# Kernel optimization log

Hardware: AMD Instinct MI355X
Metric: run time of the kernel (lower is better)

## Reference

```python
import jax, jax.numpy as jnp
import numpy as np

CDIM = 256  # part_size for energy_pooling_mask


def setup_inputs() -> dict:
    key = jax.random.key(0)
    ks = jax.random.split(key, 6)
    B, T, IDIM, HDIM, ODIM = 8, 2048, 512, 2048, 512
    x = jax.random.normal(ks[0], (B, T, IDIM), dtype=jnp.float32)
    mask_prev = jax.random.randint(ks[1], (B, T, HDIM), 0, 2, dtype=jnp.int32)
    W_enc = jax.random.normal(ks[2], (HDIM, IDIM), dtype=jnp.float32) * 0.02
    b_enc = jax.random.normal(ks[3], (HDIM,), dtype=jnp.float32) * 0.02
    W_dec = jax.random.normal(ks[4], (ODIM, HDIM), dtype=jnp.float32) * 0.02
    b_dec = jax.random.normal(ks[5], (ODIM,), dtype=jnp.float32) * 0.02
    return {"x": x, "mask_prev": mask_prev, "W_enc": W_enc, "b_enc": b_enc,
            "W_dec": W_dec, "b_dec": b_dec}


def _energy_pooling_mask(h, part_size):
    # topk over channel (last) dim of h^2; share=True -> k = 2*part_size
    B, T, H = h.shape
    k2 = 2 * part_size
    _, idx = jax.lax.top_k(h * h, k2)            # [B, T, 2c] unique indices
    idx_f = idx.reshape(B * T, k2)
    rows = jnp.arange(B * T)[:, None]
    base = jnp.zeros((B * T, H), dtype=h.dtype)
    # sum of one-hots over unique indices == scatter-set of 1.0
    mask_share = base.at[rows, idx_f].set(1.0).reshape(B, T, H)
    mask_cur = base.at[rows, idx_f[:, :part_size]].set(1.0).reshape(B, T, H)
    return mask_cur, mask_share


def reference(x, mask_prev, W_enc, b_enc, W_dec, b_dec):
    # encoder: Linear(idim -> hdim)
    h = jnp.einsum('bti,hi->bth', x, W_enc) + b_enc
    # hidden_exclude_activation with mask_prev given:
    # h[mask_prev.bool()] = 0
    mp = mask_prev.astype(h.dtype)
    h = jnp.where(mp > 0, jnp.zeros((), h.dtype), h)
    mask_cur, mask_cur_share = _energy_pooling_mask(h, CDIM)
    mask_prev_new = mp + mask_cur
    # h.masked_fill(~mask_cur_share.bool(), 0)
    h = h * mask_cur_share
    # decoder_src: Linear(hdim -> odim)
    out = jnp.einsum('bth,oh->bto', h, W_dec) + b_dec
    return out, mask_prev_new
```

## Files before the change

kernel.cpp:

```cpp
#include <hip/hip_runtime.h>
#include <hip/hip_bf16.h>

typedef __attribute__((ext_vector_type(8))) __bf16 bf16x8;
typedef __attribute__((ext_vector_type(4))) float f32x4;

#define MDIM 16384
#define HDIM 2048
#define IDIM 512
#define ODIM 512
#define CAP 768

static __device__ __forceinline__ unsigned short f2bf(float f) {
  unsigned int u = __float_as_uint(f);
  unsigned int r = (u + 0x7fffu + ((u >> 16) & 1u)) >> 16;
  return (unsigned short)r;
}

__global__ void cvt_bf16_kernel(const float* __restrict__ src,
                                unsigned short* __restrict__ dst, int n) {
  int i = (blockIdx.x * 256 + threadIdx.x) * 4;
  if (i >= n) return;
  float4 v = *(const float4*)(src + i);
  unsigned int a = (unsigned int)f2bf(v.x) | ((unsigned int)f2bf(v.y) << 16);
  unsigned int b = (unsigned int)f2bf(v.z) | ((unsigned int)f2bf(v.w) << 16);
  uint2 st; st.x = a; st.y = b;
  *(uint2*)(dst + i) = st;
}

__global__ __launch_bounds__(256) void gemm1_kernel(
    const float* __restrict__ x,
    const float* __restrict__ wenc,
    const float* __restrict__ benc,
    float* __restrict__ h) {
  __shared__ __align__(16) float As[32][132];
  __shared__ __align__(16) float Bs[32][132];
  const int t = threadIdx.x;
  const int tx = t & 15, ty = t >> 4;
  const int m0 = blockIdx.y * 128;
  const int n0 = blockIdx.x * 128;
  const int r0 = t >> 1;
  const int kh = (t & 1) * 16;

  const float* pa = x + (size_t)(m0 + r0) * IDIM + kh;
  const float* pb = wenc + (size_t)(n0 + r0) * IDIM + kh;

  float acc[8][8];
#pragma unroll
  for (int i = 0; i < 8; ++i)
#pragma unroll
    for (int j = 0; j < 8; ++j) acc[i][j] = 0.f;

  for (int kt = 0; kt < IDIM; kt += 32) {
    float4 a0 = *(const float4*)(pa + kt);
    float4 a1 = *(const float4*)(pa + kt + 4);
    float4 a2 = *(const float4*)(pa + kt + 8);
    float4 a3 = *(const float4*)(pa + kt + 12);
    float4 b0 = *(const float4*)(pb + kt);
    float4 b1 = *(const float4*)(pb + kt + 4);
    float4 b2 = *(const float4*)(pb + kt + 8);
    float4 b3 = *(const float4*)(pb + kt + 12);
    __syncthreads();
    {
      const float* aa = (const float*)&a0;
      const float av[16] = {a0.x, a0.y, a0.z, a0.w, a1.x, a1.y, a1.z, a1.w,
                            a2.x, a2.y, a2.z, a2.w, a3.x, a3.y, a3.z, a3.w};
      const float bv[16] = {b0.x, b0.y, b0.z, b0.w, b1.x, b1.y, b1.z, b1.w,
                            b2.x, b2.y, b2.z, b2.w, b3.x, b3.y, b3.z, b3.w};
      (void)aa;
#pragma unroll
      for (int j = 0; j < 16; ++j) {
        As[kh + j][r0] = av[j];
        Bs[kh + j][r0] = bv[j];
      }
    }
    __syncthreads();
#pragma unroll
    for (int k = 0; k < 32; ++k) {
      float4 av0 = *(const float4*)&As[k][ty * 4];
      float4 av1 = *(const float4*)&As[k][64 + ty * 4];
      float4 bv0 = *(const float4*)&Bs[k][tx * 4];
      float4 bv1 = *(const float4*)&Bs[k][64 + tx * 4];
      float am[8] = {av0.x, av0.y, av0.z, av0.w, av1.x, av1.y, av1.z, av1.w};
      float bm[8] = {bv0.x, bv0.y, bv0.z, bv0.w, bv1.x, bv1.y, bv1.z, bv1.w};
#pragma unroll
      for (int i = 0; i < 8; ++i)
#pragma unroll
        for (int j = 0; j < 8; ++j) acc[i][j] += am[i] * bm[j];
    }
  }
  float4 be0 = *(const float4*)(benc + n0 + tx * 4);
  float4 be1 = *(const float4*)(benc + n0 + 64 + tx * 4);
  float bb[8] = {be0.x, be0.y, be0.z, be0.w, be1.x, be1.y, be1.z, be1.w};
#pragma unroll
  for (int i = 0; i < 8; ++i) {
    int m = m0 + ((i < 4) ? (ty * 4 + i) : (64 + ty * 4 + (i - 4)));
    float* hrow = h + (size_t)m * HDIM + n0;
    float4 s0 = {acc[i][0] + bb[0], acc[i][1] + bb[1], acc[i][2] + bb[2], acc[i][3] + bb[3]};
    float4 s1 = {acc[i][4] + bb[4], acc[i][5] + bb[5], acc[i][6] + bb[6], acc[i][7] + bb[7]};
    *(float4*)(hrow + tx * 4) = s0;
    *(float4*)(hrow + 64 + tx * 4) = s1;
  }
}

__global__ __launch_bounds__(256) void select_kernel(
    float* __restrict__ hbuf,
    const int* __restrict__ maskp,
    unsigned short* __restrict__ hs) {
  const int row = blockIdx.x;
  const int t = threadIdx.x;
  const int lane = t & 63;
  const int w = t >> 6;
  __shared__ int hist[4096];
  __shared__ unsigned int cand512[CAP];
  __shared__ unsigned int cand256[CAP];
  __shared__ int scal[16];
  __shared__ int n512, n256;

  float* hrow = hbuf + (size_t)row * HDIM;
  const int* mrow = maskp + (size_t)row * HDIM;
  float hv[8];
  *(float4*)&hv[0] = *(const float4*)(hrow + t * 8);
  *(float4*)&hv[4] = *(const float4*)(hrow + t * 8 + 4);
  int4 mp0 = *(const int4*)(mrow + t * 8);
  int4 mp1 = *(const int4*)(mrow + t * 8 + 4);
  int mm[8] = {mp0.x, mp0.y, mp0.z, mp0.w, mp1.x, mp1.y, mp1.z, mp1.w};
#pragma unroll
  for (int i = 0; i < 8; ++i) hv[i] = (mm[i] > 0) ? 0.f : hv[i];
  unsigned int key[8];
#pragma unroll
  for (int i = 0; i < 8; ++i) key[i] = __float_as_uint(hv[i] * hv[i]);

#pragma unroll
  for (int i = 0; i < 16; ++i) hist[t + i * 256] = 0;
  if (t == 0) {
    n512 = 0; n256 = 0;
    scal[0] = 0; scal[1] = 0x40000000;
    scal[2] = 0; scal[3] = 0x40000000;
  }
  __syncthreads();
#pragma unroll
  for (int i = 0; i < 8; ++i)
    if (key[i]) atomicAdd(&hist[key[i] >> 20], 1);
  __syncthreads();

  if (w == 0) {
    const int base = lane * 64;
    int s = 0;
#pragma unroll
    for (int i = 0; i < 64; i += 4) {
      int4 hh = *(const int4*)&hist[base + i];
      s += hh.x + hh.y + hh.z + hh.w;
    }
    int rs = s;
#pragma unroll
    for (int d = 1; d < 64; d <<= 1) {
      int o = __shfl_down(rs, d, 64);
      rs += (lane + d < 64) ? o : 0;
    }
    int c = rs - s;
    for (int i = 60; i >= 0; i -= 4) {
      int4 hh = *(const int4*)&hist[base + i];
      int q[4] = {hh.x, hh.y, hh.z, hh.w};
#pragma unroll
      for (int j = 3; j >= 0; --j) {
        int hc = q[j];
        if (c < 512 && c + hc >= 512) { scal[0] = base + i + j; scal[1] = 512 - c; }
        if (c < 256 && c + hc >= 256) { scal[2] = base + i + j; scal[3] = 256 - c; }
        c += hc;
      }
    }
  }
  __syncthreads();
  const int b512 = scal[0], b256 = scal[2];
#pragma unroll
  for (int i = 0; i < 8; ++i) {
    if (key[i]) {
      int bin = (int)(key[i] >> 20);
      if (bin == b512) { int p = atomicAdd(&n512, 1); if (p < CAP) cand512[p] = key[i]; }
      if (bin == b256) { int p = atomicAdd(&n256, 1); if (p < CAP) cand256[p] = key[i]; }
    }
  }
  __syncthreads();

  if (w < 2) {
    const unsigned int bb = (unsigned int)scal[w * 2];
    const int r = scal[w * 2 + 1];
    const unsigned int* cand = w ? cand256 : cand512;
    int C = w ? n256 : n512;
    C = (C < CAP) ? C : CAP;
    unsigned int v = 0;
    if (r <= C) {
      v = bb << 20;
      for (int bit = 19; bit >= 0; --bit) {
        unsigned int cth = v | (1u << bit);
        int cnt = 0;
        for (int p = lane; p < C; p += 64) cnt += (cand[p] >= cth) ? 1 : 0;
#pragma unroll
        for (int d = 1; d < 64; d <<= 1) cnt += __shfl_xor(cnt, d, 64);
        if (cnt >= r) v = cth;
      }
    }
    if (lane == 0) scal[4 + w] = (int)v;
  }
  __syncthreads();
  const unsigned int v512 = (unsigned int)scal[4];
  const unsigned int v256 = (unsigned int)scal[5];

  int g = 0;
#pragma unroll
  for (int i = 0; i < 8; ++i) {
    g += (key[i] > v512) ? 1 : 0;
    g += (key[i] > v256) ? (1 << 16) : 0;
  }
#pragma unroll
  for (int d = 1; d < 64; d <<= 1) g += __shfl_xor(g, d, 64);
  if (lane == 0) scal[8 + w] = g;
  __syncthreads();
  g = scal[8] + scal[9] + scal[10] + scal[11];
  const int r512 = 512 - (g & 0xffff);
  const int r256 = 256 - (g >> 16);

  int tc = 0;
#pragma unroll
  for (int i = 0; i < 8; ++i) {
    tc += (key[i] == v512) ? 1 : 0;
    tc += (key[i] == v256) ? (1 << 16) : 0;
  }
  int sc = tc;
#pragma unroll
  for (int d = 1; d < 64; d <<= 1) {
    int o = __shfl_up(sc, d, 64);
    if (lane >= d) sc += o;
  }
  if (lane == 63) scal[12 + w] = sc;
  __syncthreads();
  int excl = sc - tc;
  for (int i = 0; i < w; ++i) excl += scal[12 + i];
  int run512 = excl & 0xffff;
  int run256 = (excl >> 16) & 0xffff;

  float mpn[8];
  unsigned int hb[4];
#pragma unroll
  for (int i = 0; i < 8; ++i) {
    bool share, cur;
    if (key[i] > v512) share = true;
    else if (key[i] == v512) { share = (run512 < r512); run512++; }
    else share = false;
    if (key[i] > v256) cur = true;
    else if (key[i] == v256) { cur = (run256 < r256); run256++; }
    else cur = false;
    mpn[i] = (float)mm[i] + (cur ? 1.0f : 0.0f);
    unsigned short bbits = f2bf(share ? hv[i] : 0.0f);
    if (i & 1) hb[i >> 1] |= ((unsigned int)bbits << 16);
    else hb[i >> 1] = (unsigned int)bbits;
  }
  float4 s0 = {mpn[0], mpn[1], mpn[2], mpn[3]};
  float4 s1 = {mpn[4], mpn[5], mpn[6], mpn[7]};
  *(float4*)(hrow + t * 8) = s0;
  *(float4*)(hrow + t * 8 + 4) = s1;
  uint4 hstore = {hb[0], hb[1], hb[2], hb[3]};
  *(uint4*)(hs + (size_t)row * HDIM + t * 8) = hstore;
}

__global__ __launch_bounds__(256) void gemm2_kernel(
    const unsigned short* __restrict__ A,
    const unsigned short* __restrict__ B,
    const float* __restrict__ bdec,
    float* __restrict__ out) {
  __shared__ __align__(16) __bf16 As[64 * 32];
  __shared__ __align__(16) __bf16 Bs[128 * 32];
  const int t = threadIdx.x;
  const int lane = t & 63;
  const int w = t >> 6;
  const int wm = w >> 1, wn = w & 1;
  const int m0 = blockIdx.y * 64;
  const int n0 = blockIdx.x * 128;
  const int r = t >> 2;
  const int k8 = (t & 3) * 8;

  f32x4 acc[2][4];
#pragma unroll
  for (int i = 0; i < 2; ++i)
#pragma unroll
    for (int j = 0; j < 4; ++j) acc[i][j] = (f32x4){0.f, 0.f, 0.f, 0.f};

  const int la = lane & 15;
  const int kq = (lane >> 4) * 8;

  for (int kt = 0; kt < HDIM; kt += 32) {
    uint4 a0 = *(const uint4*)(A + (size_t)(m0 + r) * HDIM + kt + k8);
    uint4 b0 = *(const uint4*)(B + (size_t)(n0 + r) * HDIM + kt + k8);
    uint4 b1 = *(const uint4*)(B + (size_t)(n0 + 64 + r) * HDIM + kt + k8);
    __syncthreads();
    *(uint4*)&As[r * 32 + k8] = a0;
    *(uint4*)&Bs[r * 32 + k8] = b0;
    *(uint4*)&Bs[(64 + r) * 32 + k8] = b1;
    __syncthreads();
    bf16x8 af[2], bg[4];
#pragma unroll
    for (int mi = 0; mi < 2; ++mi)
      af[mi] = *(const bf16x8*)&As[(wm * 32 + mi * 16 + la) * 32 + kq];
#pragma unroll
    for (int ni = 0; ni < 4; ++ni)
      bg[ni] = *(const bf16x8*)&Bs[(wn * 64 + ni * 16 + la) * 32 + kq];
#pragma unroll
    for (int mi = 0; mi < 2; ++mi)
#pragma unroll
      for (int ni = 0; ni < 4; ++ni)
        acc[mi][ni] = __builtin_amdgcn_mfma_f32_16x16x32_bf16(
            af[mi], bg[ni], acc[mi][ni], 0, 0, 0);
  }
  const int rq = (lane >> 4) * 4;
#pragma unroll
  for (int mi = 0; mi < 2; ++mi) {
#pragma unroll
    for (int ni = 0; ni < 4; ++ni) {
      int n = n0 + wn * 64 + ni * 16 + la;
      float bd = bdec[n];
#pragma unroll
      for (int rr = 0; rr < 4; ++rr) {
        int m = m0 + wm * 32 + mi * 16 + rq + rr;
        out[(size_t)m * ODIM + n] = acc[mi][ni][rr] + bd;
      }
    }
  }
}

extern "C" void kernel_launch(void* const* d_in, const int* in_sizes, int n_in,
                              void* d_out, int out_size, void* d_ws, size_t ws_size,
                              hipStream_t stream) {
  const float* x = (const float*)d_in[0];
  const int* mask_prev = (const int*)d_in[1];
  const float* W_enc = (const float*)d_in[2];
  const float* b_enc = (const float*)d_in[3];
  const float* W_dec = (const float*)d_in[4];
  const float* b_dec = (const float*)d_in[5];

  float* out = (float*)d_out;
  float* hbuf = out + (size_t)MDIM * ODIM;
  unsigned short* hs = (unsigned short*)d_ws;
  unsigned short* wdec = hs + (size_t)MDIM * HDIM;

  cvt_bf16_kernel<<<dim3((ODIM * HDIM) / (256 * 4)), dim3(256), 0, stream>>>(
      W_dec, wdec, ODIM * HDIM);
  gemm1_kernel<<<dim3(HDIM / 128, MDIM / 128), dim3(256), 0, stream>>>(
      x, W_enc, b_enc, hbuf);
  select_kernel<<<dim3(MDIM), dim3(256), 0, stream>>>(hbuf, mask_prev, hs);
  gemm2_kernel<<<dim3(ODIM / 128, MDIM / 64), dim3(256), 0, stream>>>(
      hs, wdec, b_dec, out);
}
```

Baseline: 837.7 us.

## Replace FP32 encoder GEMM with split-fp16 MFMA and exact-fp32 boundary refinement

Replaces the scalar FP32 SIMT encoder GEMM with an MFMA fp16 GEMM that emulates fp32 accuracy by splitting each operand into high and low fp16 parts along a concatenated K of 1536 (three products). The select kernel then finds channels whose energy lies within a small band around the top-k thresholds, recomputes those channels in exact fp32 from x and W_enc, and re-solves the thresholds so selection ties match the reference. The aim is to remove the FP32 CUDA-core bottleneck of the first GEMM. In exchange it adds two split kernels, extra workspace traffic (B_cat temporarily stored in the output buffer), and a per-row refinement step. Correctness depends on the candidate cap of 64 and on the band width.

```diff
diff --git a/kernel.cpp b/kernel.cpp
--- a/kernel.cpp
+++ b/kernel.cpp
@@ -2,13 +2,16 @@
 #include <hip/hip_bf16.h>
 
 typedef __attribute__((ext_vector_type(8))) __bf16 bf16x8;
+typedef __attribute__((ext_vector_type(8))) _Float16 f16x8;
 typedef __attribute__((ext_vector_type(4))) float f32x4;
 
 #define MDIM 16384
 #define HDIM 2048
 #define IDIM 512
 #define ODIM 512
+#define KCAT 1536
 #define CAP 768
+#define CAPC 64
 
 static __device__ __forceinline__ unsigned short f2bf(float f) {
   unsigned int u = __float_as_uint(f);
@@ -27,84 +30,131 @@
   *(uint2*)(dst + i) = st;
 }
 
-__global__ __launch_bounds__(256) void gemm1_kernel(
+static __device__ __forceinline__ void split_pack(const float4 v, uint2* h2, uint2* l2) {
+  float vv[4] = {v.x, v.y, v.z, v.w};
+  unsigned int hp[2], lp[2];
+#pragma unroll
+  for (int j = 0; j < 4; ++j) {
+    _Float16 hh = (_Float16)vv[j];
+    float back = (float)hh;
+    _Float16 ll = (_Float16)((vv[j] - back) * 2048.0f);
+    unsigned short hb = __builtin_bit_cast(unsigned short, hh);
+    unsigned short lb = __builtin_bit_cast(unsigned short, ll);
+    if (j & 1) { hp[j >> 1] |= (unsigned int)hb << 16; lp[j >> 1] |= (unsigned int)lb << 16; }
+    else       { hp[j >> 1] = hb; lp[j >> 1] = lb; }
+  }
+  h2->x = hp[0]; h2->y = hp[1];
+  l2->x = lp[0]; l2->y = lp[1];
+}
+
+__global__ void split_a_kernel(const float* __restrict__ src,
+                               unsigned short* __restrict__ dst) {
+  int idx = (blockIdx.x * 256 + threadIdx.x) * 4;
+  int row = idx >> 9, col = idx & 511;
+  uint2 h2, l2;
+  split_pack(*(const float4*)(src + idx), &h2, &l2);
+  unsigned short* drow = dst + (size_t)row * KCAT;
+  *(uint2*)(drow + col) = h2;
+  *(uint2*)(drow + 512 + col) = l2;
+  *(uint2*)(drow + 1024 + col) = h2;
+}
+
+__global__ void split_b_kernel(const float* __restrict__ src,
+                               unsigned short* __restrict__ dst) {
+  int idx = (blockIdx.x * 256 + threadIdx.x) * 4;
+  int row = idx >> 9, col = idx & 511;
+  uint2 h2, l2;
+  split_pack(*(const float4*)(src + idx), &h2, &l2);
+  unsigned short* drow = dst + (size_t)row * KCAT;
+  *(uint2*)(drow + col) = h2;
+  *(uint2*)(drow + 512 + col) = h2;
+  *(uint2*)(drow + 1024 + col) = l2;
+}
+
+__global__ __launch_bounds__(512) void gemm1_mfma_kernel(
+    const unsigned short* __restrict__ A,
+    const unsigned short* __restrict__ B,
+    const float* __restrict__ benc,
+    float* __restrict__ h) {
+  __shared__ __align__(16) _Float16 As[128 * 32];
+  __shared__ __align__(16) _Float16 Bs[128 * 32];
+  const int t = threadIdx.x;
+  const int lane = t & 63;
+  const int w = t >> 6;
+  const int wm = w >> 2;
+  const int wn = w & 3;
+  const int m0 = blockIdx.y * 128;
+  const int n0 = blockIdx.x * 128;
+  const int r = t >> 2;
+  const int k8 = (t & 3) * 8;
+
+  f32x4 acc1[4][2], acc2[4][2];
+#pragma unroll
+  for (int i = 0; i < 4; ++i)
+#pragma unroll
+    for (int j = 0; j < 2; ++j) {
+      acc1[i][j] = (f32x4){0.f, 0.f, 0.f, 0.f};
+      acc2[i][j] = (f32x4){0.f, 0.f, 0.f, 0.f};
+    }
+
+  const int la = lane & 15;
+  const int kq = (lane >> 4) * 8;
+  const unsigned short* pa = A + (size_t)(m0 + r) * KCAT + k8;
+  const unsigned short* pb = B + (size_t)(n0 + r) * KCAT + k8;
+
+  for (int kt = 0; kt < KCAT; kt += 32) {
+    uint4 av = *(const uint4*)(pa + kt);
+    uint4 bv = *(const uint4*)(pb + kt);
+    __syncthreads();
+    *(uint4*)&As[r * 32 + k8] = av;
+    *(uint4*)&Bs[r * 32 + k8] = bv;
+    __syncthreads();
+    f16x8 af[4], bg[2];
+#pragma unroll
+    for (int mi = 0; mi < 4; ++mi)
+      af[mi] = *(const f16x8*)&As[(wm * 64 + mi * 16 + la) * 32 + kq];
+#pragma unroll
+    for (int ni = 0; ni < 2; ++ni)
+      bg[ni] = *(const f16x8*)&Bs[(wn * 32 + ni * 16 + la) * 32 + kq];
+    if (kt < 512) {
+#pragma unroll
+      for (int mi = 0; mi < 4; ++mi)
+#pragma unroll
+        for (int ni = 0; ni < 2; ++ni)
+          acc1[mi][ni] = __builtin_amdgcn_mfma_f32_16x16x32_f16(
+              af[mi], bg[ni], acc1[mi][ni], 0, 0, 0);
+    } else {
+#pragma unroll
+      for (int mi = 0; mi < 4; ++mi)
+#pragma unroll
+        for (int ni = 0; ni < 2; ++ni)
+          acc2[mi][ni] = __builtin_amdgcn_mfma_f32_16x16x32_f16(
+              af[mi], bg[ni], acc2[mi][ni], 0, 0, 0);
+    }
+  }
+  const int rq = (lane >> 4) * 4;
+  const float eps = 1.0f / 2048.0f;
+#pragma unroll
+  for (int mi = 0; mi < 4; ++mi) {
+#pragma unroll
+    for (int ni = 0; ni < 2; ++ni) {
+      int n = n0 + wn * 32 + ni * 16 + la;
+      float bd = benc[n];
+#pragma unroll
+      for (int rr = 0; rr < 4; ++rr) {
+        int m = m0 + wm * 64 + mi * 16 + rq + rr;
+        h[(size_t)m * HDIM + n] = acc1[mi][ni][rr] + acc2[mi][ni][rr] * eps + bd;
+      }
+    }
+  }
+}
+
+__global__ __launch_bounds__(256) void select_kernel(
+    float* __restrict__ hbuf,
+    const int* __restrict__ maskp,
     const float* __restrict__ x,
     const float* __restrict__ wenc,
     const float* __restrict__ benc,
-    float* __restrict__ h) {
-  __shared__ __align__(16) float As[32][132];
-  __shared__ __align__(16) float Bs[32][132];
-  const int t = threadIdx.x;
-  const int tx = t & 15, ty = t >> 4;
-  const int m0 = blockIdx.y * 128;
-  const int n0 = blockIdx.x * 128;
-  const int r0 = t >> 1;
-  const int kh = (t & 1) * 16;
-
-  const float* pa = x + (size_t)(m0 + r0) * IDIM + kh;
-  const float* pb = wenc + (size_t)(n0 + r0) * IDIM + kh;
-
-  float acc[8][8];
-#pragma unroll
-  for (int i = 0; i < 8; ++i)
-#pragma unroll
-    for (int j = 0; j < 8; ++j) acc[i][j] = 0.f;
-
-  for (int kt = 0; kt < IDIM; kt += 32) {
-    float4 a0 = *(const float4*)(pa + kt);
-    float4 a1 = *(const float4*)(pa + kt + 4);
-    float4 a2 = *(const float4*)(pa + kt + 8);
-    float4 a3 = *(const float4*)(pa + kt + 12);
-    float4 b0 = *(const float4*)(pb + kt);
-    float4 b1 = *(const float4*)(pb + kt + 4);
-    float4 b2 = *(const float4*)(pb + kt + 8);
-    float4 b3 = *(const float4*)(pb + kt + 12);
-    __syncthreads();
-    {
-      const float* aa = (const float*)&a0;
-      const float av[16] = {a0.x, a0.y, a0.z, a0.w, a1.x, a1.y, a1.z, a1.w,
-                            a2.x, a2.y, a2.z, a2.w, a3.x, a3.y, a3.z, a3.w};
-      const float bv[16] = {b0.x, b0.y, b0.z, b0.w, b1.x, b1.y, b1.z, b1.w,
-                            b2.x, b2.y, b2.z, b2.w, b3.x, b3.y, b3.z, b3.w};
-      (void)aa;
-#pragma unroll
-      for (int j = 0; j < 16; ++j) {
-        As[kh + j][r0] = av[j];
-        Bs[kh + j][r0] = bv[j];
-      }
-    }
-    __syncthreads();
-#pragma unroll
-    for (int k = 0; k < 32; ++k) {
-      float4 av0 = *(const float4*)&As[k][ty * 4];
-      float4 av1 = *(const float4*)&As[k][64 + ty * 4];
-      float4 bv0 = *(const float4*)&Bs[k][tx * 4];
-      float4 bv1 = *(const float4*)&Bs[k][64 + tx * 4];
-      float am[8] = {av0.x, av0.y, av0.z, av0.w, av1.x, av1.y, av1.z, av1.w};
-      float bm[8] = {bv0.x, bv0.y, bv0.z, bv0.w, bv1.x, bv1.y, bv1.z, bv1.w};
-#pragma unroll
-      for (int i = 0; i < 8; ++i)
-#pragma unroll
-        for (int j = 0; j < 8; ++j) acc[i][j] += am[i] * bm[j];
-    }
-  }
-  float4 be0 = *(const float4*)(benc + n0 + tx * 4);
-  float4 be1 = *(const float4*)(benc + n0 + 64 + tx * 4);
-  float bb[8] = {be0.x, be0.y, be0.z, be0.w, be1.x, be1.y, be1.z, be1.w};
-#pragma unroll
-  for (int i = 0; i < 8; ++i) {
-    int m = m0 + ((i < 4) ? (ty * 4 + i) : (64 + ty * 4 + (i - 4)));
-    float* hrow = h + (size_t)m * HDIM + n0;
-    float4 s0 = {acc[i][0] + bb[0], acc[i][1] + bb[1], acc[i][2] + bb[2], acc[i][3] + bb[3]};
-    float4 s1 = {acc[i][4] + bb[4], acc[i][5] + bb[5], acc[i][6] + bb[6], acc[i][7] + bb[7]};
-    *(float4*)(hrow + tx * 4) = s0;
-    *(float4*)(hrow + 64 + tx * 4) = s1;
-  }
-}
-
-__global__ __launch_bounds__(256) void select_kernel(
-    float* __restrict__ hbuf,
-    const int* __restrict__ maskp,
     unsigned short* __restrict__ hs) {
   const int row = blockIdx.x;
   const int t = threadIdx.x;
@@ -113,8 +163,11 @@
   __shared__ int hist[4096];
   __shared__ unsigned int cand512[CAP];
   __shared__ unsigned int cand256[CAP];
-  __shared__ int scal[16];
-  __shared__ int n512, n256;
+  __shared__ float xrow[IDIM];
+  __shared__ int cidx[2][CAPC];
+  __shared__ float cex[2][CAPC];
+  __shared__ int scal[24];
+  __shared__ int n512, n256, ncnt0, ncnt1;
 
   float* hrow = hbuf + (size_t)row * HDIM;
   const int* mrow = maskp + (size_t)row * HDIM;
@@ -130,10 +183,12 @@
 #pragma unroll
   for (int i = 0; i < 8; ++i) key[i] = __float_as_uint(hv[i] * hv[i]);
 
+  *(float2*)&xrow[t * 2] = *(const float2*)(x + (size_t)row * IDIM + t * 2);
+
 #pragma unroll
   for (int i = 0; i < 16; ++i) hist[t + i * 256] = 0;
   if (t == 0) {
-    n512 = 0; n256 = 0;
+    n512 = 0; n256 = 0; ncnt0 = 0; ncnt1 = 0;
     scal[0] = 0; scal[1] = 0x40000000;
     scal[2] = 0; scal[3] = 0x40000000;
   }
@@ -203,8 +258,81 @@
     if (lane == 0) scal[4 + w] = (int)v;
   }
   __syncthreads();
+  const unsigned int v512a = (unsigned int)scal[4];
+  const unsigned int v256a = (unsigned int)scal[5];
+
+  const float vf0 = __uint_as_float(v512a), vf1 = __uint_as_float(v256a);
+  const bool act0 = (v512a != 0), act1 = (v256a != 0);
+  const float wd0 = 1e-4f * sqrtf(vf0) + 1e-12f;
+  const float wd1 = 1e-4f * sqrtf(vf1) + 1e-12f;
+  const float hi0 = vf0 + wd0, lo0 = vf0 - wd0;
+  const float hi1 = vf1 + wd1, lo1 = vf1 - wd1;
+  int gf = 0;
+#pragma unroll
+  for (int i = 0; i < 8; ++i) {
+    float kf = __uint_as_float(key[i]);
+    if (act0) {
+      if (kf > hi0) gf += 1;
+      else if (kf >= lo0) { int p = atomicAdd(&ncnt0, 1); if (p < CAPC) cidx[0][p] = t * 8 + i; }
+    }
+    if (act1) {
+      if (kf > hi1) gf += (1 << 16);
+      else if (kf >= lo1) { int p = atomicAdd(&ncnt1, 1); if (p < CAPC) cidx[1][p] = t * 8 + i; }
+    }
+  }
+#pragma unroll
+  for (int d = 1; d < 64; d <<= 1) gf += __shfl_xor(gf, d, 64);
+  if (lane == 0) scal[16 + w] = gf;
+  __syncthreads();
+  const int gft = scal[16] + scal[17] + scal[18] + scal[19];
+  const int t0n = (ncnt0 < CAPC) ? ncnt0 : CAPC;
+  const int t1n = (ncnt1 < CAPC) ? ncnt1 : CAPC;
+
+  if (w < 2) {
+    const int n = w ? t1n : t0n;
+    if (lane < n) {
+      const int ch = cidx[w][lane];
+      const float* wr = wenc + (size_t)ch * IDIM;
+      float s = 0.f;
+      for (int k = 0; k < IDIM; ++k) s = fmaf(xrow[k], wr[k], s);
+      cex[w][lane] = s + benc[ch];
+    }
+  }
+  __syncthreads();
+
+  if (w < 2) {
+    const bool act = w ? act1 : act0;
+    const int n = w ? t1n : t0n;
+    if (act && n > 0) {
+      int rr = (w ? 256 : 512) - (w ? (gft >> 16) : (gft & 0xffff));
+      rr = (rr < 1) ? 1 : ((rr > n) ? n : rr);
+      unsigned int v = 0;
+      for (int b = 31; b >= 0; --b) {
+        unsigned int cth = v | (1u << b);
+        int cnt = 0;
+        for (int j = lane; j < n; j += 64) {
+          float q = cex[w][j];
+          cnt += (__float_as_uint(q * q) >= cth) ? 1 : 0;
+        }
+#pragma unroll
+        for (int d = 1; d < 64; d <<= 1) cnt += __shfl_xor(cnt, d, 64);
+        if (cnt >= rr) v = cth;
+      }
+      if (lane == 0) scal[4 + w] = (int)v;
+    }
+  }
+  __syncthreads();
   const unsigned int v512 = (unsigned int)scal[4];
   const unsigned int v256 = (unsigned int)scal[5];
+
+  for (int j = 0; j < t0n; ++j) {
+    int ch = cidx[0][j];
+    if ((ch >> 3) == t) { float e = cex[0][j]; hv[ch & 7] = e; key[ch & 7] = __float_as_uint(e * e); }
+  }
+  for (int j = 0; j < t1n; ++j) {
+    int ch = cidx[1][j];
+    if ((ch >> 3) == t) { float e = cex[1][j]; hv[ch & 7] = e; key[ch & 7] = __float_as_uint(e * e); }
+  }
 
   int g = 0;
 #pragma unroll
@@ -339,14 +467,19 @@
 
   float* out = (float*)d_out;
   float* hbuf = out + (size_t)MDIM * ODIM;
+  unsigned short* acat = (unsigned short*)d_ws;
   unsigned short* hs = (unsigned short*)d_ws;
   unsigned short* wdec = hs + (size_t)MDIM * HDIM;
-
-  cvt_bf16_kernel<<<dim3((ODIM * HDIM) / (256 * 4)), dim3(256), 0, stream>>>(
+  unsigned short* bcat = (unsigned short*)d_out;
+
+  split_a_kernel<<<dim3((MDIM * IDIM) / 1024), dim3(256), 0, stream>>>(x, acat);
+  split_b_kernel<<<dim3((HDIM * IDIM) / 1024), dim3(256), 0, stream>>>(W_enc, bcat);
+  cvt_bf16_kernel<<<dim3((ODIM * HDIM) / 1024), dim3(256), 0, stream>>>(
       W_dec, wdec, ODIM * HDIM);
-  gemm1_kernel<<<dim3(HDIM / 128, MDIM / 128), dim3(256), 0, stream>>>(
-      x, W_enc, b_enc, hbuf);
-  select_kernel<<<dim3(MDIM), dim3(256), 0, stream>>>(hbuf, mask_prev, hs);
+  gemm1_mfma_kernel<<<dim3(HDIM / 128, MDIM / 128), dim3(512), 0, stream>>>(
+      acat, bcat, b_enc, hbuf);
+  select_kernel<<<dim3(MDIM), dim3(256), 0, stream>>>(
+      hbuf, mask_prev, x, W_enc, b_enc, hs);
   gemm2_kernel<<<dim3(ODIM / 128, MDIM / 64), dim3(256), 0, stream>>>(
       hs, wdec, b_dec, out);
 }
```

Measured after the change: 963.6 us. 15.0% more time.
